# Optimization experiments

Hardware: AMD Instinct MI355X
Metric: run time of the kernel (lower is better)

The kernel has to match this reference:

```python
import jax, jax.numpy as jnp
import numpy as np
from jax import lax

INPUT, HIDDEN, OUT = 64, 128, 40
B, T = 256, 512


def _lstm_layer(x, Wih, Whh, bih, bhh):
    # x: [B, T, D]; PyTorch gate order: i, f, g, o in stacked [4H, .] weights
    Bsz = x.shape[0]
    H = Whh.shape[1]
    b = bih + bhh

    def step(carry, xt):
        h, c = carry
        gates = xt @ Wih.T + h @ Whh.T + b  # [B, 4H]
        i, f, g, o = jnp.split(gates, 4, axis=-1)
        i = jax.nn.sigmoid(i)
        f = jax.nn.sigmoid(f)
        g = jnp.tanh(g)
        o = jax.nn.sigmoid(o)
        c = f * c + i * g
        h = o * jnp.tanh(c)
        return (h, c), h

    init = (jnp.zeros((Bsz, H), x.dtype), jnp.zeros((Bsz, H), x.dtype))
    (h_last, _), ys = lax.scan(step, init, jnp.swapaxes(x, 0, 1))
    return jnp.swapaxes(ys, 0, 1), h_last


def setup_inputs() -> dict:
    key = jax.random.key(0)
    ks = jax.random.split(key, 11)
    s_in = 1.0 / np.sqrt(HIDDEN)
    u = lambda k, shp: jax.random.uniform(k, shp, jnp.float32, -s_in, s_in)
    return {
        "x": jax.random.normal(ks[0], (B, T, INPUT), jnp.float32),
        "Wih0": u(ks[1], (4 * HIDDEN, INPUT)),
        "Whh0": u(ks[2], (4 * HIDDEN, HIDDEN)),
        "bih0": u(ks[3], (4 * HIDDEN,)),
        "bhh0": u(ks[4], (4 * HIDDEN,)),
        "Wih1": u(ks[5], (4 * HIDDEN, HIDDEN)),
        "Whh1": u(ks[6], (4 * HIDDEN, HIDDEN)),
        "bih1": u(ks[7], (4 * HIDDEN,)),
        "bhh1": u(ks[8], (4 * HIDDEN,)),
        "Wfc": u(ks[9], (OUT, HIDDEN)),
        "bfc": u(ks[10], (OUT,)),
    }


def reference(x, Wih0, Whh0, bih0, bhh0, Wih1, Whh1, bih1, bhh1, Wfc, bfc):
    y0, _ = _lstm_layer(x, Wih0, Whh0, bih0, bhh0)        # [B, T, H]
    _, h_last = _lstm_layer(y0, Wih1, Whh1, bih1, bhh1)   # [B, H] == y[:, -1]
    return h_last @ Wfc.T + bfc                            # [B, 40]
```

## Files before the change

### kernel.cpp

```cpp
#include <hip/hip_runtime.h>

#define BATCH 256
#define TLEN  512
#define DIN   64
#define HID   128
#define NOUT  40
#define SC    16

typedef _Float16 f16x8 __attribute__((ext_vector_type(8)));
typedef float    f32x4 __attribute__((ext_vector_type(4)));

#define MFMA16(a, b, c) __builtin_amdgcn_mfma_f32_16x16x32_f16((a), (b), (c), 0, 0, 0)

#define BARRIER() do {                                      \
    asm volatile("s_waitcnt lgkmcnt(0)" ::: "memory");      \
    __builtin_amdgcn_s_barrier();                           \
} while (0)

static __device__ __forceinline__ f16x8 pack8(float4 a, float4 b) {
    f16x8 v;
    v[0] = (_Float16)a.x; v[1] = (_Float16)a.y; v[2] = (_Float16)a.z; v[3] = (_Float16)a.w;
    v[4] = (_Float16)b.x; v[5] = (_Float16)b.y; v[6] = (_Float16)b.z; v[7] = (_Float16)b.w;
    return v;
}
static __device__ __forceinline__ float sig_(float x) {
    return __builtin_amdgcn_rcpf(1.0f + __expf(-x));
}
static __device__ __forceinline__ float tanh_(float x) {
    return fmaf(-2.0f, __builtin_amdgcn_rcpf(__expf(2.0f * x) + 1.0f), 1.0f);
}
static __device__ __forceinline__ f32x4 splat4(float v) { return (f32x4){v, v, v, v}; }

#define LD8(base, g, K, kt) pack8(*(const float4*)((base) + (size_t)(g) * (K) + (kt) * 32 + kg * 8), \
                                  *(const float4*)((base) + (size_t)(g) * (K) + (kt) * 32 + kg * 8 + 4))

#define H_STEP_CORE(SL, P)                                                      \
    f32x4 xi = *(const f32x4*)&xacc[((SL) * HID + hid) * 4];                    \
    const _Float16* hb = &h_lds[P][0];                                          \
    f16x8 h0 = *(const f16x8*)(hb + kg * 8);                                    \
    f16x8 h1 = *(const f16x8*)(hb + 32 + kg * 8);                               \
    f16x8 h2 = *(const f16x8*)(hb + 64 + kg * 8);                               \
    f16x8 h3 = *(const f16x8*)(hb + 96 + kg * 8);                               \
    f32x4 a0 = MFMA16(h0, Wh00, xi);                                            \
    f32x4 a1 = MFMA16(h0, Wh10, splat4(xi[1]));                                 \
    f32x4 a2 = MFMA16(h0, Wh20, splat4(xi[2]));                                 \
    f32x4 a3 = MFMA16(h0, Wh30, splat4(xi[3]));                                 \
    a0 = MFMA16(h1, Wh01, a0); a1 = MFMA16(h1, Wh11, a1);                       \
    a2 = MFMA16(h1, Wh21, a2); a3 = MFMA16(h1, Wh31, a3);                       \
    a0 = MFMA16(h2, Wh02, a0); a1 = MFMA16(h2, Wh12, a1);                       \
    a2 = MFMA16(h2, Wh22, a2); a3 = MFMA16(h2, Wh32, a3);                       \
    a0 = MFMA16(h3, Wh03, a0); a1 = MFMA16(h3, Wh13, a1);                       \
    a2 = MFMA16(h3, Wh23, a2); a3 = MFMA16(h3, Wh33, a3);                       \
    float iv = sig_(a0[0]), fv = sig_(a1[0]);                                   \
    float gv = tanh_(a2[0]), ov = sig_(a3[0]);                                  \
    cc = fmaf(fv, cc, iv * gv);                                                 \
    hv = ov * tanh_(cc);

__global__ void __attribute__((amdgpu_flat_work_group_size(512, 512), amdgpu_waves_per_eu(2, 2)))
lstm_l0(const float* __restrict__ x,
        const float* __restrict__ Wih, const float* __restrict__ Whh,
        const float* __restrict__ bih, const float* __restrict__ bhh,
        float* __restrict__ hstate, float* __restrict__ cstate,
        _Float16* __restrict__ y0, int t0, int t1)
{
    const int b    = blockIdx.x;
    const int tid  = threadIdx.x;
    const int lane = tid & 63;
    const int wave = tid >> 6;
    const int col  = lane & 15, kg = lane >> 4;
    const int hid  = wave * 16 + col;

    __shared__ __align__(16) float    xacc[SC * HID * 4];
    __shared__ __align__(16) _Float16 h_lds[2][HID];

    f16x8 Wx00 = LD8(Wih, 0 * HID + hid, DIN, 0), Wx01 = LD8(Wih, 0 * HID + hid, DIN, 1);
    f16x8 Wx10 = LD8(Wih, 1 * HID + hid, DIN, 0), Wx11 = LD8(Wih, 1 * HID + hid, DIN, 1);
    f16x8 Wx20 = LD8(Wih, 2 * HID + hid, DIN, 0), Wx21 = LD8(Wih, 2 * HID + hid, DIN, 1);
    f16x8 Wx30 = LD8(Wih, 3 * HID + hid, DIN, 0), Wx31 = LD8(Wih, 3 * HID + hid, DIN, 1);
    f16x8 Wh00 = LD8(Whh, 0 * HID + hid, HID, 0), Wh01 = LD8(Whh, 0 * HID + hid, HID, 1);
    f16x8 Wh02 = LD8(Whh, 0 * HID + hid, HID, 2), Wh03 = LD8(Whh, 0 * HID + hid, HID, 3);
    f16x8 Wh10 = LD8(Whh, 1 * HID + hid, HID, 0), Wh11 = LD8(Whh, 1 * HID + hid, HID, 1);
    f16x8 Wh12 = LD8(Whh, 1 * HID + hid, HID, 2), Wh13 = LD8(Whh, 1 * HID + hid, HID, 3);
    f16x8 Wh20 = LD8(Whh, 2 * HID + hid, HID, 0), Wh21 = LD8(Whh, 2 * HID + hid, HID, 1);
    f16x8 Wh22 = LD8(Whh, 2 * HID + hid, HID, 2), Wh23 = LD8(Whh, 2 * HID + hid, HID, 3);
    f16x8 Wh30 = LD8(Whh, 3 * HID + hid, HID, 0), Wh31 = LD8(Whh, 3 * HID + hid, HID, 1);
    f16x8 Wh32 = LD8(Whh, 3 * HID + hid, HID, 2), Wh33 = LD8(Whh, 3 * HID + hid, HID, 3);
    asm("" : "+a"(Wx00), "+a"(Wx01), "+a"(Wx10), "+a"(Wx11),
             "+a"(Wx20), "+a"(Wx21), "+a"(Wx30), "+a"(Wx31));
    asm("" : "+a"(Wh00), "+a"(Wh01), "+a"(Wh02), "+a"(Wh03),
             "+a"(Wh10), "+a"(Wh11), "+a"(Wh12), "+a"(Wh13));
    asm("" : "+a"(Wh20), "+a"(Wh21), "+a"(Wh22), "+a"(Wh23),
             "+a"(Wh30), "+a"(Wh31), "+a"(Wh32), "+a"(Wh33));

    const float bs0 = bih[0 * HID + hid] + bhh[0 * HID + hid];
    const float bs1 = bih[1 * HID + hid] + bhh[1 * HID + hid];
    const float bs2 = bih[2 * HID + hid] + bhh[2 * HID + hid];
    const float bs3 = bih[3 * HID + hid] + bhh[3 * HID + hid];

    float cc = cstate[(size_t)b * HID + hid];
    float hv = hstate[(size_t)b * HID + hid];
    if (kg == 0) h_lds[0][hid] = (_Float16)hv;

    const float* xA = x + (size_t)b * TLEN * DIN + (size_t)col * DIN + kg * 8;
    _Float16* y0p = y0 + (size_t)b * HID + hid;

    const int nt = t1 - t0;
    for (int sc = 0; sc < nt; sc += SC) {
        {
            const float* pa = xA + (size_t)(t0 + sc) * DIN;
            f16x8 A0 = pack8(*(const float4*)pa,        *(const float4*)(pa + 4));
            f16x8 A1 = pack8(*(const float4*)(pa + 32), *(const float4*)(pa + 36));
            f32x4 g0 = splat4(bs0), g1 = splat4(bs1), g2 = splat4(bs2), g3 = splat4(bs3);
            g0 = MFMA16(A0, Wx00, g0); g1 = MFMA16(A0, Wx10, g1);
            g2 = MFMA16(A0, Wx20, g2); g3 = MFMA16(A0, Wx30, g3);
            g0 = MFMA16(A1, Wx01, g0); g1 = MFMA16(A1, Wx11, g1);
            g2 = MFMA16(A1, Wx21, g2); g3 = MFMA16(A1, Wx31, g3);
            #pragma unroll
            for (int r = 0; r < 4; ++r) {
                const int tl = kg * 4 + r;
                float* d = &xacc[(tl * HID + hid) * 4];
                d[0] = g0[r]; d[1] = g1[r]; d[2] = g2[r]; d[3] = g3[r];
            }
        }
        BARRIER();
        for (int s = 0; s < SC; s += 2) {
            {
                H_STEP_CORE(s, 0)
                if (kg == 0) {
                    h_lds[1][hid] = (_Float16)hv;
                    y0p[(size_t)(sc + s) * (BATCH * HID)] = (_Float16)hv;
                }
                BARRIER();
            }
            {
                H_STEP_CORE(s + 1, 1)
                if (kg == 0) {
                    h_lds[0][hid] = (_Float16)hv;
                    y0p[(size_t)(sc + s + 1) * (BATCH * HID)] = (_Float16)hv;
                }
                BARRIER();
            }
        }
    }
    if (kg == 0) {
        cstate[(size_t)b * HID + hid] = cc;
        hstate[(size_t)b * HID + hid] = hv;
    }
}

__global__ void __attribute__((amdgpu_flat_work_group_size(512, 512), amdgpu_waves_per_eu(2, 2)))
lstm_l1(const _Float16* __restrict__ y0in,
        const float* __restrict__ Wih, const float* __restrict__ Whh,
        const float* __restrict__ bih, const float* __restrict__ bhh,
        float* __restrict__ hstate, float* __restrict__ cstate,
        int t0, int t1)
{
    const int b    = blockIdx.x;
    const int tid  = threadIdx.x;
    const int lane = tid & 63;
    const int wave = tid >> 6;
    const int col  = lane & 15, kg = lane >> 4;
    const int hid  = wave * 16 + col;

    __shared__ __align__(16) float    xacc[SC * HID * 4];
    __shared__ __align__(16) _Float16 h_lds[2][HID];

    f16x8 Wh00 = LD8(Whh, 0 * HID + hid, HID, 0), Wh01 = LD8(Whh, 0 * HID + hid, HID, 1);
    f16x8 Wh02 = LD8(Whh, 0 * HID + hid, HID, 2), Wh03 = LD8(Whh, 0 * HID + hid, HID, 3);
    f16x8 Wh10 = LD8(Whh, 1 * HID + hid, HID, 0), Wh11 = LD8(Whh, 1 * HID + hid, HID, 1);
    f16x8 Wh12 = LD8(Whh, 1 * HID + hid, HID, 2), Wh13 = LD8(Whh, 1 * HID + hid, HID, 3);
    f16x8 Wh20 = LD8(Whh, 2 * HID + hid, HID, 0), Wh21 = LD8(Whh, 2 * HID + hid, HID, 1);
    f16x8 Wh22 = LD8(Whh, 2 * HID + hid, HID, 2), Wh23 = LD8(Whh, 2 * HID + hid, HID, 3);
    f16x8 Wh30 = LD8(Whh, 3 * HID + hid, HID, 0), Wh31 = LD8(Whh, 3 * HID + hid, HID, 1);
    f16x8 Wh32 = LD8(Whh, 3 * HID + hid, HID, 2), Wh33 = LD8(Whh, 3 * HID + hid, HID, 3);
    asm("" : "+a"(Wh00), "+a"(Wh01), "+a"(Wh02), "+a"(Wh03),
             "+a"(Wh10), "+a"(Wh11), "+a"(Wh12), "+a"(Wh13));
    asm("" : "+a"(Wh20), "+a"(Wh21), "+a"(Wh22), "+a"(Wh23),
             "+a"(Wh30), "+a"(Wh31), "+a"(Wh32), "+a"(Wh33));

    const float bs0 = bih[0 * HID + hid] + bhh[0 * HID + hid];
    const float bs1 = bih[1 * HID + hid] + bhh[1 * HID + hid];
    const float bs2 = bih[2 * HID + hid] + bhh[2 * HID + hid];
    const float bs3 = bih[3 * HID + hid] + bhh[3 * HID + hid];

    float cc = cstate[(size_t)b * HID + hid];
    float hv = hstate[(size_t)b * HID + hid];
    if (kg == 0) h_lds[0][hid] = (_Float16)hv;

    const _Float16* yA = y0in + ((size_t)col * BATCH + b) * HID + kg * 8;

    const int nt = t1 - t0;
    for (int sc = 0; sc < nt; sc += SC) {
        {
            f16x8 Wy00 = LD8(Wih, 0 * HID + hid, HID, 0), Wy01 = LD8(Wih, 0 * HID + hid, HID, 1);
            f16x8 Wy02 = LD8(Wih, 0 * HID + hid, HID, 2), Wy03 = LD8(Wih, 0 * HID + hid, HID, 3);
            f16x8 Wy10 = LD8(Wih, 1 * HID + hid, HID, 0), Wy11 = LD8(Wih, 1 * HID + hid, HID, 1);
            f16x8 Wy12 = LD8(Wih, 1 * HID + hid, HID, 2), Wy13 = LD8(Wih, 1 * HID + hid, HID, 3);
            f16x8 Wy20 = LD8(Wih, 2 * HID + hid, HID, 0), Wy21 = LD8(Wih, 2 * HID + hid, HID, 1);
            f16x8 Wy22 = LD8(Wih, 2 * HID + hid, HID, 2), Wy23 = LD8(Wih, 2 * HID + hid, HID, 3);
            f16x8 Wy30 = LD8(Wih, 3 * HID + hid, HID, 0), Wy31 = LD8(Wih, 3 * HID + hid, HID, 1);
            f16x8 Wy32 = LD8(Wih, 3 * HID + hid, HID, 2), Wy33 = LD8(Wih, 3 * HID + hid, HID, 3);
            const _Float16* pa = yA + (size_t)sc * (BATCH * HID);
            f16x8 A0 = *(const f16x8*)(pa);
            f16x8 A1 = *(const f16x8*)(pa + 32);
            f16x8 A2 = *(const f16x8*)(pa + 64);
            f16x8 A3 = *(const f16x8*)(pa + 96);
            f32x4 g0 = splat4(bs0), g1 = splat4(bs1), g2 = splat4(bs2), g3 = splat4(bs3);
            g0 = MFMA16(A0, Wy00, g0); g1 = MFMA16(A0, Wy10, g1);
            g2 = MFMA16(A0, Wy20, g2); g3 = MFMA16(A0, Wy30, g3);
            g0 = MFMA16(A1, Wy01, g0); g1 = MFMA16(A1, Wy11, g1);
            g2 = MFMA16(A1, Wy21, g2); g3 = MFMA16(A1, Wy31, g3);
            g0 = MFMA16(A2, Wy02, g0); g1 = MFMA16(A2, Wy12, g1);
            g2 = MFMA16(A2, Wy22, g2); g3 = MFMA16(A2, Wy32, g3);
            g0 = MFMA16(A3, Wy03, g0); g1 = MFMA16(A3, Wy13, g1);
            g2 = MFMA16(A3, Wy23, g2); g3 = MFMA16(A3, Wy33, g3);
            #pragma unroll
            for (int r = 0; r < 4; ++r) {
                const int tl = kg * 4 + r;
                float* d = &xacc[(tl * HID + hid) * 4];
                d[0] = g0[r]; d[1] = g1[r]; d[2] = g2[r]; d[3] = g3[r];
            }
        }
        BARRIER();
        for (int s = 0; s < SC; s += 2) {
            {
                H_STEP_CORE(s, 0)
                if (kg == 0) h_lds[1][hid] = (_Float16)hv;
                BARRIER();
            }
            {
                H_STEP_CORE(s + 1, 1)
                if (kg == 0) h_lds[0][hid] = (_Float16)hv;
                BARRIER();
            }
        }
    }
    if (kg == 0) {
        cstate[(size_t)b * HID + hid] = cc;
        hstate[(size_t)b * HID + hid] = hv;
    }
}

__global__ __launch_bounds__(128) void fc_kernel(
    const float* __restrict__ h1, const float* __restrict__ Wfc,
    const float* __restrict__ bfc, float* __restrict__ out)
{
    const int b = blockIdx.x;
    const int o = threadIdx.x;
    __shared__ float hs[HID];
    hs[o] = h1[(size_t)b * HID + o];
    __syncthreads();
    if (o < NOUT) {
        const float4* w  = reinterpret_cast<const float4*>(Wfc + (size_t)o * HID);
        const float4* hv = reinterpret_cast<const float4*>(hs);
        float acc = bfc[o];
        #pragma unroll
        for (int q = 0; q < HID / 4; ++q) {
            float4 wv = w[q]; float4 h4 = hv[q];
            acc = fmaf(wv.x, h4.x, fmaf(wv.y, h4.y, fmaf(wv.z, h4.z, fmaf(wv.w, h4.w, acc))));
        }
        out[(size_t)b * NOUT + o] = acc;
    }
}

extern "C" void kernel_launch(void* const* d_in, const int* in_sizes, int n_in,
                              void* d_out, int out_size, void* d_ws, size_t ws_size,
                              hipStream_t stream) {
    const float* x    = (const float*)d_in[0];
    const float* Wih0 = (const float*)d_in[1];
    const float* Whh0 = (const float*)d_in[2];
    const float* bih0 = (const float*)d_in[3];
    const float* bhh0 = (const float*)d_in[4];
    const float* Wih1 = (const float*)d_in[5];
    const float* Whh1 = (const float*)d_in[6];
    const float* bih1 = (const float*)d_in[7];
    const float* bhh1 = (const float*)d_in[8];
    const float* Wfc  = (const float*)d_in[9];
    const float* bfc  = (const float*)d_in[10];
    float* out = (float*)d_out;

    float* hst0 = (float*)d_ws;
    float* cst0 = hst0 + BATCH * HID;
    float* hst1 = cst0 + BATCH * HID;
    float* cst1 = hst1 + BATCH * HID;
    _Float16* y0 = (_Float16*)(cst1 + BATCH * HID);

    const size_t stateBytes = (size_t)4 * BATCH * HID * sizeof(float);
    size_t avail = ws_size > stateBytes ? ws_size - stateBytes : 0;
    int Tc = (int)(avail / ((size_t)BATCH * HID * 2));
    if (Tc > TLEN) Tc = TLEN;
    Tc &= ~(SC - 1);
    if (Tc < SC) Tc = SC;

    hipMemsetAsync(d_ws, 0, stateBytes, stream);

    for (int t0 = 0; t0 < TLEN; t0 += Tc) {
        int t1 = t0 + Tc; if (t1 > TLEN) t1 = TLEN;
        lstm_l0<<<BATCH, 512, 0, stream>>>(x, Wih0, Whh0, bih0, bhh0, hst0, cst0, y0, t0, t1);
        lstm_l1<<<BATCH, 512, 0, stream>>>(y0, Wih1, Whh1, bih1, bhh1, hst1, cst1, t0, t1);
    }
    fc_kernel<<<BATCH, 128, 0, stream>>>(hst1, Wfc, bfc, out);
}
```

Measured before the change: 578.3 us.

## Fuse both LSTM layers and FC into one wavefront-pipelined kernel

Replaces the separate layer-0 and layer-1 kernels and the FC kernel with one kernel per batch row. Layer 1 runs one chunk behind layer 0, reading layer-0 outputs from a double-buffered LDS buffer instead of global memory, and both recurrences share each step's barrier. This removes the global y0 round-trip, the memset, and extra launches, and halves the count of serial barrier steps. In exchange it holds both recurrent weight sets in registers, raising register pressure, adds more LDS, and reloads the input-projection weights from global memory every chunk.

```diff
diff --git a/kernel.cpp b/kernel.cpp
--- a/kernel.cpp
+++ b/kernel.cpp
@@ -6,6 +6,7 @@
 #define HID   128
 #define NOUT  40
 #define SC    16
+#define NCH   (TLEN / SC)
 
 typedef _Float16 f16x8 __attribute__((ext_vector_type(8)));
 typedef float    f32x4 __attribute__((ext_vector_type(4)));
@@ -34,232 +35,223 @@
 #define LD8(base, g, K, kt) pack8(*(const float4*)((base) + (size_t)(g) * (K) + (kt) * 32 + kg * 8), \
                                   *(const float4*)((base) + (size_t)(g) * (K) + (kt) * 32 + kg * 8 + 4))
 
-#define H_STEP_CORE(SL, P)                                                      \
-    f32x4 xi = *(const f32x4*)&xacc[((SL) * HID + hid) * 4];                    \
-    const _Float16* hb = &h_lds[P][0];                                          \
-    f16x8 h0 = *(const f16x8*)(hb + kg * 8);                                    \
-    f16x8 h1 = *(const f16x8*)(hb + 32 + kg * 8);                               \
-    f16x8 h2 = *(const f16x8*)(hb + 64 + kg * 8);                               \
-    f16x8 h3 = *(const f16x8*)(hb + 96 + kg * 8);                               \
-    f32x4 a0 = MFMA16(h0, Wh00, xi);                                            \
-    f32x4 a1 = MFMA16(h0, Wh10, splat4(xi[1]));                                 \
-    f32x4 a2 = MFMA16(h0, Wh20, splat4(xi[2]));                                 \
-    f32x4 a3 = MFMA16(h0, Wh30, splat4(xi[3]));                                 \
-    a0 = MFMA16(h1, Wh01, a0); a1 = MFMA16(h1, Wh11, a1);                       \
-    a2 = MFMA16(h1, Wh21, a2); a3 = MFMA16(h1, Wh31, a3);                       \
-    a0 = MFMA16(h2, Wh02, a0); a1 = MFMA16(h2, Wh12, a1);                       \
-    a2 = MFMA16(h2, Wh22, a2); a3 = MFMA16(h2, Wh32, a3);                       \
-    a0 = MFMA16(h3, Wh03, a0); a1 = MFMA16(h3, Wh13, a1);                       \
-    a2 = MFMA16(h3, Wh23, a2); a3 = MFMA16(h3, Wh33, a3);                       \
-    float iv = sig_(a0[0]), fv = sig_(a1[0]);                                   \
-    float gv = tanh_(a2[0]), ov = sig_(a3[0]);                                  \
-    cc = fmaf(fv, cc, iv * gv);                                                 \
-    hv = ov * tanh_(cc);
-
 __global__ void __attribute__((amdgpu_flat_work_group_size(512, 512), amdgpu_waves_per_eu(2, 2)))
-lstm_l0(const float* __restrict__ x,
-        const float* __restrict__ Wih, const float* __restrict__ Whh,
-        const float* __restrict__ bih, const float* __restrict__ bhh,
-        float* __restrict__ hstate, float* __restrict__ cstate,
-        _Float16* __restrict__ y0, int t0, int t1)
+lstm_fused(const float* __restrict__ x,
+           const float* __restrict__ Wih0, const float* __restrict__ Whh0,
+           const float* __restrict__ bih0, const float* __restrict__ bhh0,
+           const float* __restrict__ Wih1, const float* __restrict__ Whh1,
+           const float* __restrict__ bih1, const float* __restrict__ bhh1,
+           const float* __restrict__ Wfc,  const float* __restrict__ bfc,
+           float* __restrict__ out)
 {
     const int b    = blockIdx.x;
     const int tid  = threadIdx.x;
-    const int lane = tid & 63;
-    const int wave = tid >> 6;
+    const int lane = tid & 63, wave = tid >> 6;
     const int col  = lane & 15, kg = lane >> 4;
     const int hid  = wave * 16 + col;
 
     __shared__ __align__(16) float    xacc[SC * HID * 4];
-    __shared__ __align__(16) _Float16 h_lds[2][HID];
-
-    f16x8 Wx00 = LD8(Wih, 0 * HID + hid, DIN, 0), Wx01 = LD8(Wih, 0 * HID + hid, DIN, 1);
-    f16x8 Wx10 = LD8(Wih, 1 * HID + hid, DIN, 0), Wx11 = LD8(Wih, 1 * HID + hid, DIN, 1);
-    f16x8 Wx20 = LD8(Wih, 2 * HID + hid, DIN, 0), Wx21 = LD8(Wih, 2 * HID + hid, DIN, 1);
-    f16x8 Wx30 = LD8(Wih, 3 * HID + hid, DIN, 0), Wx31 = LD8(Wih, 3 * HID + hid, DIN, 1);
-    f16x8 Wh00 = LD8(Whh, 0 * HID + hid, HID, 0), Wh01 = LD8(Whh, 0 * HID + hid, HID, 1);
-    f16x8 Wh02 = LD8(Whh, 0 * HID + hid, HID, 2), Wh03 = LD8(Whh, 0 * HID + hid, HID, 3);
-    f16x8 Wh10 = LD8(Whh, 1 * HID + hid, HID, 0), Wh11 = LD8(Whh, 1 * HID + hid, HID, 1);
-    f16x8 Wh12 = LD8(Whh, 1 * HID + hid, HID, 2), Wh13 = LD8(Whh, 1 * HID + hid, HID, 3);
-    f16x8 Wh20 = LD8(Whh, 2 * HID + hid, HID, 0), Wh21 = LD8(Whh, 2 * HID + hid, HID, 1);
-    f16x8 Wh22 = LD8(Whh, 2 * HID + hid, HID, 2), Wh23 = LD8(Whh, 2 * HID + hid, HID, 3);
-    f16x8 Wh30 = LD8(Whh, 3 * HID + hid, HID, 0), Wh31 = LD8(Whh, 3 * HID + hid, HID, 1);
-    f16x8 Wh32 = LD8(Whh, 3 * HID + hid, HID, 2), Wh33 = LD8(Whh, 3 * HID + hid, HID, 3);
-    asm("" : "+a"(Wx00), "+a"(Wx01), "+a"(Wx10), "+a"(Wx11),
-             "+a"(Wx20), "+a"(Wx21), "+a"(Wx30), "+a"(Wx31));
-    asm("" : "+a"(Wh00), "+a"(Wh01), "+a"(Wh02), "+a"(Wh03),
-             "+a"(Wh10), "+a"(Wh11), "+a"(Wh12), "+a"(Wh13));
-    asm("" : "+a"(Wh20), "+a"(Wh21), "+a"(Wh22), "+a"(Wh23),
-             "+a"(Wh30), "+a"(Wh31), "+a"(Wh32), "+a"(Wh33));
-
-    const float bs0 = bih[0 * HID + hid] + bhh[0 * HID + hid];
-    const float bs1 = bih[1 * HID + hid] + bhh[1 * HID + hid];
-    const float bs2 = bih[2 * HID + hid] + bhh[2 * HID + hid];
-    const float bs3 = bih[3 * HID + hid] + bhh[3 * HID + hid];
-
-    float cc = cstate[(size_t)b * HID + hid];
-    float hv = hstate[(size_t)b * HID + hid];
-    if (kg == 0) h_lds[0][hid] = (_Float16)hv;
+    __shared__ __align__(16) float    yacc[SC * HID * 4];
+    __shared__ __align__(16) _Float16 h0_lds[2][HID];
+    __shared__ __align__(16) _Float16 h1_lds[2][HID];
+    __shared__ __align__(16) _Float16 y0buf[2][SC][HID];
+
+    f16x8 Wh0_00 = LD8(Whh0, 0 * HID + hid, HID, 0), Wh0_01 = LD8(Whh0, 0 * HID + hid, HID, 1);
+    f16x8 Wh0_02 = LD8(Whh0, 0 * HID + hid, HID, 2), Wh0_03 = LD8(Whh0, 0 * HID + hid, HID, 3);
+    f16x8 Wh0_10 = LD8(Whh0, 1 * HID + hid, HID, 0), Wh0_11 = LD8(Whh0, 1 * HID + hid, HID, 1);
+    f16x8 Wh0_12 = LD8(Whh0, 1 * HID + hid, HID, 2), Wh0_13 = LD8(Whh0, 1 * HID + hid, HID, 3);
+    f16x8 Wh0_20 = LD8(Whh0, 2 * HID + hid, HID, 0), Wh0_21 = LD8(Whh0, 2 * HID + hid, HID, 1);
+    f16x8 Wh0_22 = LD8(Whh0, 2 * HID + hid, HID, 2), Wh0_23 = LD8(Whh0, 2 * HID + hid, HID, 3);
+    f16x8 Wh0_30 = LD8(Whh0, 3 * HID + hid, HID, 0), Wh0_31 = LD8(Whh0, 3 * HID + hid, HID, 1);
+    f16x8 Wh0_32 = LD8(Whh0, 3 * HID + hid, HID, 2), Wh0_33 = LD8(Whh0, 3 * HID + hid, HID, 3);
+    f16x8 Wh1_00 = LD8(Whh1, 0 * HID + hid, HID, 0), Wh1_01 = LD8(Whh1, 0 * HID + hid, HID, 1);
+    f16x8 Wh1_02 = LD8(Whh1, 0 * HID + hid, HID, 2), Wh1_03 = LD8(Whh1, 0 * HID + hid, HID, 3);
+    f16x8 Wh1_10 = LD8(Whh1, 1 * HID + hid, HID, 0), Wh1_11 = LD8(Whh1, 1 * HID + hid, HID, 1);
+    f16x8 Wh1_12 = LD8(Whh1, 1 * HID + hid, HID, 2), Wh1_13 = LD8(Whh1, 1 * HID + hid, HID, 3);
+    f16x8 Wh1_20 = LD8(Whh1, 2 * HID + hid, HID, 0), Wh1_21 = LD8(Whh1, 2 * HID + hid, HID, 1);
+    f16x8 Wh1_22 = LD8(Whh1, 2 * HID + hid, HID, 2), Wh1_23 = LD8(Whh1, 2 * HID + hid, HID, 3);
+    f16x8 Wh1_30 = LD8(Whh1, 3 * HID + hid, HID, 0), Wh1_31 = LD8(Whh1, 3 * HID + hid, HID, 1);
+    f16x8 Wh1_32 = LD8(Whh1, 3 * HID + hid, HID, 2), Wh1_33 = LD8(Whh1, 3 * HID + hid, HID, 3);
+    asm("" : "+a"(Wh0_00), "+a"(Wh0_01), "+a"(Wh0_02), "+a"(Wh0_03),
+             "+a"(Wh0_10), "+a"(Wh0_11), "+a"(Wh0_12), "+a"(Wh0_13));
+    asm("" : "+a"(Wh0_20), "+a"(Wh0_21), "+a"(Wh0_22), "+a"(Wh0_23),
+             "+a"(Wh0_30), "+a"(Wh0_31), "+a"(Wh0_32), "+a"(Wh0_33));
+    asm("" : "+a"(Wh1_00), "+a"(Wh1_01), "+a"(Wh1_02), "+a"(Wh1_03),
+             "+a"(Wh1_10), "+a"(Wh1_11), "+a"(Wh1_12), "+a"(Wh1_13));
+    asm("" : "+a"(Wh1_20), "+a"(Wh1_21), "+a"(Wh1_22), "+a"(Wh1_23),
+             "+a"(Wh1_30), "+a"(Wh1_31), "+a"(Wh1_32), "+a"(Wh1_33));
+
+    const float bs00 = bih0[0 * HID + hid] + bhh0[0 * HID + hid];
+    const float bs01 = bih0[1 * HID + hid] + bhh0[1 * HID + hid];
+    const float bs02 = bih0[2 * HID + hid] + bhh0[2 * HID + hid];
+    const float bs03 = bih0[3 * HID + hid] + bhh0[3 * HID + hid];
+    const float bs10 = bih1[0 * HID + hid] + bhh1[0 * HID + hid];
+    const float bs11 = bih1[1 * HID + hid] + bhh1[1 * HID + hid];
+    const float bs12 = bih1[2 * HID + hid] + bhh1[2 * HID + hid];
+    const float bs13 = bih1[3 * HID + hid] + bhh1[3 * HID + hid];
+
+    float cc0 = 0.f, hv0 = 0.f, cc1 = 0.f, hv1 = 0.f;
+    if (kg == 0) { h0_lds[0][hid] = (_Float16)0.f; h1_lds[0][hid] = (_Float16)0.f; }
 
     const float* xA = x + (size_t)b * TLEN * DIN + (size_t)col * DIN + kg * 8;
-    _Float16* y0p = y0 + (size_t)b * HID + hid;
-
-    const int nt = t1 - t0;
-    for (int sc = 0; sc < nt; sc += SC) {
-        {
-            const float* pa = xA + (size_t)(t0 + sc) * DIN;
-            f16x8 A0 = pack8(*(const float4*)pa,        *(const float4*)(pa + 4));
-            f16x8 A1 = pack8(*(const float4*)(pa + 32), *(const float4*)(pa + 36));
-            f32x4 g0 = splat4(bs0), g1 = splat4(bs1), g2 = splat4(bs2), g3 = splat4(bs3);
-            g0 = MFMA16(A0, Wx00, g0); g1 = MFMA16(A0, Wx10, g1);
-            g2 = MFMA16(A0, Wx20, g2); g3 = MFMA16(A0, Wx30, g3);
-            g0 = MFMA16(A1, Wx01, g0); g1 = MFMA16(A1, Wx11, g1);
-            g2 = MFMA16(A1, Wx21, g2); g3 = MFMA16(A1, Wx31, g3);
-            #pragma unroll
-            for (int r = 0; r < 4; ++r) {
-                const int tl = kg * 4 + r;
-                float* d = &xacc[(tl * HID + hid) * 4];
-                d[0] = g0[r]; d[1] = g1[r]; d[2] = g2[r]; d[3] = g3[r];
-            }
+
+#define XPROJ(C) do {                                                            \
+    f16x8 Wx00 = LD8(Wih0, 0 * HID + hid, DIN, 0), Wx01 = LD8(Wih0, 0 * HID + hid, DIN, 1); \
+    f16x8 Wx10 = LD8(Wih0, 1 * HID + hid, DIN, 0), Wx11 = LD8(Wih0, 1 * HID + hid, DIN, 1); \
+    f16x8 Wx20 = LD8(Wih0, 2 * HID + hid, DIN, 0), Wx21 = LD8(Wih0, 2 * HID + hid, DIN, 1); \
+    f16x8 Wx30 = LD8(Wih0, 3 * HID + hid, DIN, 0), Wx31 = LD8(Wih0, 3 * HID + hid, DIN, 1); \
+    const float* pa = xA + (size_t)(C) * SC * DIN;                               \
+    f16x8 A0 = pack8(*(const float4*)pa,        *(const float4*)(pa + 4));       \
+    f16x8 A1 = pack8(*(const float4*)(pa + 32), *(const float4*)(pa + 36));      \
+    f32x4 g0 = splat4(bs00), g1 = splat4(bs01), g2 = splat4(bs02), g3 = splat4(bs03); \
+    g0 = MFMA16(A0, Wx00, g0); g1 = MFMA16(A0, Wx10, g1);                        \
+    g2 = MFMA16(A0, Wx20, g2); g3 = MFMA16(A0, Wx30, g3);                        \
+    g0 = MFMA16(A1, Wx01, g0); g1 = MFMA16(A1, Wx11, g1);                        \
+    g2 = MFMA16(A1, Wx21, g2); g3 = MFMA16(A1, Wx31, g3);                        \
+    _Pragma("unroll") for (int r = 0; r < 4; ++r) {                              \
+        float* d = &xacc[((kg * 4 + r) * HID + hid) * 4];                        \
+        d[0] = g0[r]; d[1] = g1[r]; d[2] = g2[r]; d[3] = g3[r];                  \
+    }                                                                            \
+} while (0)
+
+#define YPROJ(C) do {                                                            \
+    f16x8 Wy00 = LD8(Wih1, 0 * HID + hid, HID, 0), Wy01 = LD8(Wih1, 0 * HID + hid, HID, 1); \
+    f16x8 Wy02 = LD8(Wih1, 0 * HID + hid, HID, 2), Wy03 = LD8(Wih1, 0 * HID + hid, HID, 3); \
+    f16x8 Wy10 = LD8(Wih1, 1 * HID + hid, HID, 0), Wy11 = LD8(Wih1, 1 * HID + hid, HID, 1); \
+    f16x8 Wy12 = LD8(Wih1, 1 * HID + hid, HID, 2), Wy13 = LD8(Wih1, 1 * HID + hid, HID, 3); \
+    f16x8 Wy20 = LD8(Wih1, 2 * HID + hid, HID, 0), Wy21 = LD8(Wih1, 2 * HID + hid, HID, 1); \
+    f16x8 Wy22 = LD8(Wih1, 2 * HID + hid, HID, 2), Wy23 = LD8(Wih1, 2 * HID + hid, HID, 3); \
+    f16x8 Wy30 = LD8(Wih1, 3 * HID + hid, HID, 0), Wy31 = LD8(Wih1, 3 * HID + hid, HID, 1); \
+    f16x8 Wy32 = LD8(Wih1, 3 * HID + hid, HID, 2), Wy33 = LD8(Wih1, 3 * HID + hid, HID, 3); \
+    const _Float16* pa = &y0buf[((C) - 1) & 1][col][kg * 8];                     \
+    f16x8 A0 = *(const f16x8*)pa;                                                \
+    f16x8 A1 = *(const f16x8*)(pa + 32);                                         \
+    f16x8 A2 = *(const f16x8*)(pa + 64);                                         \
+    f16x8 A3 = *(const f16x8*)(pa + 96);                                         \
+    f32x4 g0 = splat4(bs10), g1 = splat4(bs11), g2 = splat4(bs12), g3 = splat4(bs13); \
+    g0 = MFMA16(A0, Wy00, g0); g1 = MFMA16(A0, Wy10, g1);                        \
+    g2 = MFMA16(A0, Wy20, g2); g3 = MFMA16(A0, Wy30, g3);                        \
+    g0 = MFMA16(A1, Wy01, g0); g1 = MFMA16(A1, Wy11, g1);                        \
+    g2 = MFMA16(A1, Wy21, g2); g3 = MFMA16(A1, Wy31, g3);                        \
+    g0 = MFMA16(A2, Wy02, g0); g1 = MFMA16(A2, Wy12, g1);                        \
+    g2 = MFMA16(A2, Wy22, g2); g3 = MFMA16(A2, Wy32, g3);                        \
+    g0 = MFMA16(A3, Wy03, g0); g1 = MFMA16(A3, Wy13, g1);                        \
+    g2 = MFMA16(A3, Wy23, g2); g3 = MFMA16(A3, Wy33, g3);                        \
+    _Pragma("unroll") for (int r = 0; r < 4; ++r) {                              \
+        float* d = &yacc[((kg * 4 + r) * HID + hid) * 4];                        \
+        d[0] = g0[r]; d[1] = g1[r]; d[2] = g2[r]; d[3] = g3[r];                  \
+    }                                                                            \
+} while (0)
+
+#define L0_PART(S, P, YB)                                                        \
+    f32x4 xi = *(const f32x4*)&xacc[((S) * HID + hid) * 4];                      \
+    const _Float16* h0b = &h0_lds[P][0];                                         \
+    f16x8 p00 = *(const f16x8*)(h0b + kg * 8);                                   \
+    f16x8 p01 = *(const f16x8*)(h0b + 32 + kg * 8);                              \
+    f16x8 p02 = *(const f16x8*)(h0b + 64 + kg * 8);                              \
+    f16x8 p03 = *(const f16x8*)(h0b + 96 + kg * 8);                              \
+    f32x4 a00 = MFMA16(p00, Wh0_00, xi);                                         \
+    f32x4 a01 = MFMA16(p00, Wh0_10, splat4(xi[1]));                              \
+    f32x4 a02 = MFMA16(p00, Wh0_20, splat4(xi[2]));                              \
+    f32x4 a03 = MFMA16(p00, Wh0_30, splat4(xi[3]));                              \
+    a00 = MFMA16(p01, Wh0_01, a00); a01 = MFMA16(p01, Wh0_11, a01);              \
+    a02 = MFMA16(p01, Wh0_21, a02); a03 = MFMA16(p01, Wh0_31, a03);              \
+    a00 = MFMA16(p02, Wh0_02, a00); a01 = MFMA16(p02, Wh0_12, a01);              \
+    a02 = MFMA16(p02, Wh0_22, a02); a03 = MFMA16(p02, Wh0_32, a03);              \
+    a00 = MFMA16(p03, Wh0_03, a00); a01 = MFMA16(p03, Wh0_13, a01);              \
+    a02 = MFMA16(p03, Wh0_23, a02); a03 = MFMA16(p03, Wh0_33, a03);
+
+#define L0_FINISH(S, P, YB)                                                      \
+    float iv0 = sig_(a00[0]), fv0 = sig_(a01[0]);                                \
+    float gv0 = tanh_(a02[0]), ov0 = sig_(a03[0]);                               \
+    cc0 = fmaf(fv0, cc0, iv0 * gv0);                                             \
+    hv0 = ov0 * tanh_(cc0);                                                      \
+    if (kg == 0) {                                                               \
+        _Float16 hh0 = (_Float16)hv0;                                            \
+        h0_lds[(P) ^ 1][hid] = hh0;                                              \
+        y0buf[YB][S][hid]    = hh0;                                              \
+    }
+
+#define L1_PART(S, P)                                                            \
+    f32x4 yi = *(const f32x4*)&yacc[((S) * HID + hid) * 4];                      \
+    const _Float16* h1b = &h1_lds[P][0];                                         \
+    f16x8 q00 = *(const f16x8*)(h1b + kg * 8);                                   \
+    f16x8 q01 = *(const f16x8*)(h1b + 32 + kg * 8);                              \
+    f16x8 q02 = *(const f16x8*)(h1b + 64 + kg * 8);                              \
+    f16x8 q03 = *(const f16x8*)(h1b + 96 + kg * 8);                              \
+    f32x4 a10 = MFMA16(q00, Wh1_00, yi);                                         \
+    f32x4 a11 = MFMA16(q00, Wh1_10, splat4(yi[1]));                              \
+    f32x4 a12 = MFMA16(q00, Wh1_20, splat4(yi[2]));                              \
+    f32x4 a13 = MFMA16(q00, Wh1_30, splat4(yi[3]));                              \
+    a10 = MFMA16(q01, Wh1_01, a10); a11 = MFMA16(q01, Wh1_11, a11);              \
+    a12 = MFMA16(q01, Wh1_21, a12); a13 = MFMA16(q01, Wh1_31, a13);              \
+    a10 = MFMA16(q02, Wh1_02, a10); a11 = MFMA16(q02, Wh1_12, a11);              \
+    a12 = MFMA16(q02, Wh1_22, a12); a13 = MFMA16(q02, Wh1_32, a13);              \
+    a10 = MFMA16(q03, Wh1_03, a10); a11 = MFMA16(q03, Wh1_13, a11);              \
+    a12 = MFMA16(q03, Wh1_23, a12); a13 = MFMA16(q03, Wh1_33, a13);
+
+#define L1_FINISH(P)                                                             \
+    float iv1 = sig_(a10[0]), fv1 = sig_(a11[0]);                                \
+    float gv1 = tanh_(a12[0]), ov1 = sig_(a13[0]);                               \
+    cc1 = fmaf(fv1, cc1, iv1 * gv1);                                             \
+    hv1 = ov1 * tanh_(cc1);                                                      \
+    if (kg == 0) h1_lds[(P) ^ 1][hid] = (_Float16)hv1;
+
+#define STEP_BOTH(S, P, YB) do {                                                 \
+    L0_PART(S, P, YB)                                                            \
+    L1_PART(S, P)                                                                \
+    L0_FINISH(S, P, YB)                                                          \
+    L1_FINISH(P)                                                                 \
+    BARRIER();                                                                   \
+} while (0)
+
+#define STEP_L0(S, P, YB) do {                                                   \
+    L0_PART(S, P, YB)                                                            \
+    L0_FINISH(S, P, YB)                                                          \
+    BARRIER();                                                                   \
+} while (0)
+
+#define STEP_L1(S, P) do {                                                       \
+    L1_PART(S, P)                                                                \
+    L1_FINISH(P)                                                                 \
+    BARRIER();                                                                   \
+} while (0)
+
+    XPROJ(0);
+    BARRIER();
+    for (int s = 0; s < SC; s += 2) {
+        STEP_L0(s,     0, 0);
+        STEP_L0(s + 1, 1, 0);
+    }
+    for (int c = 1; c < NCH; ++c) {
+        XPROJ(c);
+        YPROJ(c);
+        BARRIER();
+        const int yb = c & 1;
+        for (int s = 0; s < SC; s += 2) {
+            STEP_BOTH(s,     0, yb);
+            STEP_BOTH(s + 1, 1, yb);
         }
-        BARRIER();
-        for (int s = 0; s < SC; s += 2) {
-            {
-                H_STEP_CORE(s, 0)
-                if (kg == 0) {
-                    h_lds[1][hid] = (_Float16)hv;
-                    y0p[(size_t)(sc + s) * (BATCH * HID)] = (_Float16)hv;
-                }
-                BARRIER();
-            }
-            {
-                H_STEP_CORE(s + 1, 1)
-                if (kg == 0) {
-                    h_lds[0][hid] = (_Float16)hv;
-                    y0p[(size_t)(sc + s + 1) * (BATCH * HID)] = (_Float16)hv;
-                }
-                BARRIER();
-            }
-        }
-    }
-    if (kg == 0) {
-        cstate[(size_t)b * HID + hid] = cc;
-        hstate[(size_t)b * HID + hid] = hv;
-    }
-}
-
-__global__ void __attribute__((amdgpu_flat_work_group_size(512, 512), amdgpu_waves_per_eu(2, 2)))
-lstm_l1(const _Float16* __restrict__ y0in,
-        const float* __restrict__ Wih, const float* __restrict__ Whh,
-        const float* __restrict__ bih, const float* __restrict__ bhh,
-        float* __restrict__ hstate, float* __restrict__ cstate,
-        int t0, int t1)
-{
-    const int b    = blockIdx.x;
-    const int tid  = threadIdx.x;
-    const int lane = tid & 63;
-    const int wave = tid >> 6;
-    const int col  = lane & 15, kg = lane >> 4;
-    const int hid  = wave * 16 + col;
-
-    __shared__ __align__(16) float    xacc[SC * HID * 4];
-    __shared__ __align__(16) _Float16 h_lds[2][HID];
-
-    f16x8 Wh00 = LD8(Whh, 0 * HID + hid, HID, 0), Wh01 = LD8(Whh, 0 * HID + hid, HID, 1);
-    f16x8 Wh02 = LD8(Whh, 0 * HID + hid, HID, 2), Wh03 = LD8(Whh, 0 * HID + hid, HID, 3);
-    f16x8 Wh10 = LD8(Whh, 1 * HID + hid, HID, 0), Wh11 = LD8(Whh, 1 * HID + hid, HID, 1);
-    f16x8 Wh12 = LD8(Whh, 1 * HID + hid, HID, 2), Wh13 = LD8(Whh, 1 * HID + hid, HID, 3);
-    f16x8 Wh20 = LD8(Whh, 2 * HID + hid, HID, 0), Wh21 = LD8(Whh, 2 * HID + hid, HID, 1);
-    f16x8 Wh22 = LD8(Whh, 2 * HID + hid, HID, 2), Wh23 = LD8(Whh, 2 * HID + hid, HID, 3);
-    f16x8 Wh30 = LD8(Whh, 3 * HID + hid, HID, 0), Wh31 = LD8(Whh, 3 * HID + hid, HID, 1);
-    f16x8 Wh32 = LD8(Whh, 3 * HID + hid, HID, 2), Wh33 = LD8(Whh, 3 * HID + hid, HID, 3);
-    asm("" : "+a"(Wh00), "+a"(Wh01), "+a"(Wh02), "+a"(Wh03),
-             "+a"(Wh10), "+a"(Wh11), "+a"(Wh12), "+a"(Wh13));
-    asm("" : "+a"(Wh20), "+a"(Wh21), "+a"(Wh22), "+a"(Wh23),
-             "+a"(Wh30), "+a"(Wh31), "+a"(Wh32), "+a"(Wh33));
-
-    const float bs0 = bih[0 * HID + hid] + bhh[0 * HID + hid];
-    const float bs1 = bih[1 * HID + hid] + bhh[1 * HID + hid];
-    const float bs2 = bih[2 * HID + hid] + bhh[2 * HID + hid];
-    const float bs3 = bih[3 * HID + hid] + bhh[3 * HID + hid];
-
-    float cc = cstate[(size_t)b * HID + hid];
-    float hv = hstate[(size_t)b * HID + hid];
-    if (kg == 0) h_lds[0][hid] = (_Float16)hv;
-
-    const _Float16* yA = y0in + ((size_t)col * BATCH + b) * HID + kg * 8;
-
-    const int nt = t1 - t0;
-    for (int sc = 0; sc < nt; sc += SC) {
-        {
-            f16x8 Wy00 = LD8(Wih, 0 * HID + hid, HID, 0), Wy01 = LD8(Wih, 0 * HID + hid, HID, 1);
-            f16x8 Wy02 = LD8(Wih, 0 * HID + hid, HID, 2), Wy03 = LD8(Wih, 0 * HID + hid, HID, 3);
-            f16x8 Wy10 = LD8(Wih, 1 * HID + hid, HID, 0), Wy11 = LD8(Wih, 1 * HID + hid, HID, 1);
-            f16x8 Wy12 = LD8(Wih, 1 * HID + hid, HID, 2), Wy13 = LD8(Wih, 1 * HID + hid, HID, 3);
-            f16x8 Wy20 = LD8(Wih, 2 * HID + hid, HID, 0), Wy21 = LD8(Wih, 2 * HID + hid, HID, 1);
-            f16x8 Wy22 = LD8(Wih, 2 * HID + hid, HID, 2), Wy23 = LD8(Wih, 2 * HID + hid, HID, 3);
-            f16x8 Wy30 = LD8(Wih, 3 * HID + hid, HID, 0), Wy31 = LD8(Wih, 3 * HID + hid, HID, 1);
-            f16x8 Wy32 = LD8(Wih, 3 * HID + hid, HID, 2), Wy33 = LD8(Wih, 3 * HID + hid, HID, 3);
-            const _Float16* pa = yA + (size_t)sc * (BATCH * HID);
-            f16x8 A0 = *(const f16x8*)(pa);
-            f16x8 A1 = *(const f16x8*)(pa + 32);
-            f16x8 A2 = *(const f16x8*)(pa + 64);
-            f16x8 A3 = *(const f16x8*)(pa + 96);
-            f32x4 g0 = splat4(bs0), g1 = splat4(bs1), g2 = splat4(bs2), g3 = splat4(bs3);
-            g0 = MFMA16(A0, Wy00, g0); g1 = MFMA16(A0, Wy10, g1);
-            g2 = MFMA16(A0, Wy20, g2); g3 = MFMA16(A0, Wy30, g3);
-            g0 = MFMA16(A1, Wy01, g0); g1 = MFMA16(A1, Wy11, g1);
-            g2 = MFMA16(A1, Wy21, g2); g3 = MFMA16(A1, Wy31, g3);
-            g0 = MFMA16(A2, Wy02, g0); g1 = MFMA16(A2, Wy12, g1);
-            g2 = MFMA16(A2, Wy22, g2); g3 = MFMA16(A2, Wy32, g3);
-            g0 = MFMA16(A3, Wy03, g0); g1 = MFMA16(A3, Wy13, g1);
-            g2 = MFMA16(A3, Wy23, g2); g3 = MFMA16(A3, Wy33, g3);
-            #pragma unroll
-            for (int r = 0; r < 4; ++r) {
-                const int tl = kg * 4 + r;
-                float* d = &xacc[(tl * HID + hid) * 4];
-                d[0] = g0[r]; d[1] = g1[r]; d[2] = g2[r]; d[3] = g3[r];
-            }
-        }
-        BARRIER();
-        for (int s = 0; s < SC; s += 2) {
-            {
-                H_STEP_CORE(s, 0)
-                if (kg == 0) h_lds[1][hid] = (_Float16)hv;
-                BARRIER();
-            }
-            {
-                H_STEP_CORE(s + 1, 1)
-                if (kg == 0) h_lds[0][hid] = (_Float16)hv;
-                BARRIER();
-            }
-        }
-    }
-    if (kg == 0) {
-        cstate[(size_t)b * HID + hid] = cc;
-        hstate[(size_t)b * HID + hid] = hv;
-    }
-}
-
-__global__ __launch_bounds__(128) void fc_kernel(
-    const float* __restrict__ h1, const float* __restrict__ Wfc,
-    const float* __restrict__ bfc, float* __restrict__ out)
-{
-    const int b = blockIdx.x;
-    const int o = threadIdx.x;
-    __shared__ float hs[HID];
-    hs[o] = h1[(size_t)b * HID + o];
-    __syncthreads();
-    if (o < NOUT) {
-        const float4* w  = reinterpret_cast<const float4*>(Wfc + (size_t)o * HID);
-        const float4* hv = reinterpret_cast<const float4*>(hs);
-        float acc = bfc[o];
+    }
+    YPROJ(NCH);
+    BARRIER();
+    for (int s = 0; s < SC; s += 2) {
+        STEP_L1(s,     0);
+        STEP_L1(s + 1, 1);
+    }
+
+    if (kg == 0) xacc[hid] = hv1;
+    BARRIER();
+    if (tid < NOUT) {
+        const float4* w  = (const float4*)(Wfc + (size_t)tid * HID);
+        const float4* hvv = (const float4*)xacc;
+        float acc = bfc[tid];
         #pragma unroll
         for (int q = 0; q < HID / 4; ++q) {
-            float4 wv = w[q]; float4 h4 = hv[q];
+            float4 wv = w[q]; float4 h4 = hvv[q];
             acc = fmaf(wv.x, h4.x, fmaf(wv.y, h4.y, fmaf(wv.z, h4.z, fmaf(wv.w, h4.w, acc))));
         }
-        out[(size_t)b * NOUT + o] = acc;
+        out[(size_t)b * NOUT + tid] = acc;
     }
 }
 
@@ -279,25 +271,6 @@
     const float* bfc  = (const float*)d_in[10];
     float* out = (float*)d_out;
 
-    float* hst0 = (float*)d_ws;
-    float* cst0 = hst0 + BATCH * HID;
-    float* hst1 = cst0 + BATCH * HID;
-    float* cst1 = hst1 + BATCH * HID;
-    _Float16* y0 = (_Float16*)(cst1 + BATCH * HID);
-
-    const size_t stateBytes = (size_t)4 * BATCH * HID * sizeof(float);
-    size_t avail = ws_size > stateBytes ? ws_size - stateBytes : 0;
-    int Tc = (int)(avail / ((size_t)BATCH * HID * 2));
-    if (Tc > TLEN) Tc = TLEN;
-    Tc &= ~(SC - 1);
-    if (Tc < SC) Tc = SC;
-
-    hipMemsetAsync(d_ws, 0, stateBytes, stream);
-
-    for (int t0 = 0; t0 < TLEN; t0 += Tc) {
-        int t1 = t0 + Tc; if (t1 > TLEN) t1 = TLEN;
-        lstm_l0<<<BATCH, 512, 0, stream>>>(x, Wih0, Whh0, bih0, bhh0, hst0, cst0, y0, t0, t1);
-        lstm_l1<<<BATCH, 512, 0, stream>>>(y0, Wih1, Whh1, bih1, bhh1, hst1, cst1, t0, t1);
-    }
-    fc_kernel<<<BATCH, 128, 0, stream>>>(hst1, Wfc, bfc, out);
-}
+    lstm_fused<<<BATCH, 512, 0, stream>>>(x, Wih0, Whh0, bih0, bhh0,
+                                          Wih1, Whh1, bih1, bhh1, Wfc, bfc, out);
+}
```

Result: slower. 724.8 us (+25.3%).
